# Kernel tuning notes

Hardware: AMD Instinct MI355X
Metric: run time of the kernel (lower is better)

## Reference

```python
import jax, jax.numpy as jnp
import numpy as np

BETA = 0.25


def setup_inputs() -> dict:
    key = jax.random.key(0)
    k1, k2 = jax.random.split(key)
    z = jax.random.normal(k1, (16, 64, 32, 32), dtype=jnp.float32)
    emb_w = jax.random.normal(k2, (16384, 64), dtype=jnp.float32)
    return {"z": z, "emb_w": emb_w}


def reference(z, emb_w):
    # z: [b, c, h, w] with c == embed_dim; emb_w: [n_embed, embed_dim]
    b, c, h, w = z.shape
    zc = jnp.transpose(z, (0, 2, 3, 1))          # [b, h, w, c]
    zf = zc.reshape(-1, c)                        # [N, c]
    # squared euclidean distances: ||z||^2 - 2 z E^T + ||E||^2  -> [N, n_embed]
    d = (jnp.sum(zf * zf, axis=1, keepdims=True)
         - 2.0 * (zf @ emb_w.T)
         + jnp.sum(emb_w * emb_w, axis=1))
    idx = jnp.argmin(d, axis=1)                   # [N]
    z_q = emb_w[idx].reshape(zc.shape)            # [b, h, w, c]
    # commitment loss (codebook side detached, eval-mode forward)
    loss = BETA * jnp.mean((jax.lax.stop_gradient(z_q) - zc) ** 2)
    # straight-through estimator
    z_q_ste = zc + jax.lax.stop_gradient(z_q - zc)
    z_q_out = jnp.transpose(z_q_ste, (0, 3, 1, 2))  # back to bchw
    return (z_q_out, loss)
```

## Files before the change

kernel.cpp:

```cpp
#include <hip/hip_runtime.h>
#include <math.h>

#define NQ      16384
#define NE      16384
#define DIM     64
#define QB      256
#define CS1     8
#define CPB1    (NE / CS1)
#define CPW1    (CPB1 / 4)
#define NT1     (CPW1 / 32)
#define THREADS 256
#define EPS     0.4f

typedef _Float16 half8  __attribute__((ext_vector_type(8)));
typedef float    f32x4  __attribute__((ext_vector_type(4)));
typedef float    f32x16 __attribute__((ext_vector_type(16)));
typedef unsigned int       uint32;
typedef unsigned short     uint16;
typedef unsigned long long uint64;

typedef union { f32x16 v; f32x4 q[4]; } nvec16;

#define W_NORMS   0
#define W_PM1     16384
#define W_PM2     147456
#define W_PG      278528
#define W_FINALG  344064
#define W_RLIST   360448
#define W_COUNT   376832
#define W_LOSSP   376848
#define W_RKEY    377104
#define W_ZH1     409872
#define W_ZH2     934160
#define W_EH1     1458448
#define W_EH2     1982736

__device__ inline uint32 fmono(float f) {
    uint32 u = __float_as_uint(f);
    return (u & 0x80000000u) ? ~u : (u | 0x80000000u);
}

__global__ __launch_bounds__(THREADS)
void vq_prep(const float* __restrict__ z, const float* __restrict__ emb,
             _Float16* __restrict__ zh1, _Float16* __restrict__ zh2,
             _Float16* __restrict__ eh1, _Float16* __restrict__ eh2,
             float* __restrict__ norms, uint32* __restrict__ count) {
    if (blockIdx.x == 0 && threadIdx.x == 0) *count = 0u;
    if (blockIdx.x < 64) {
        int e = blockIdx.x * THREADS + threadIdx.x;
        const float4* row = reinterpret_cast<const float4*>(emb + (size_t)e * DIM);
        float s = 0.f;
#pragma unroll
        for (int i = 0; i < DIM / 4; ++i) {
            float4 v = row[i];
            s = fmaf(v.x, v.x, s); s = fmaf(v.y, v.y, s);
            s = fmaf(v.z, v.z, s); s = fmaf(v.w, v.w, s);
            union { _Float16 h[4]; uint2 u; } p1, p2;
            float f[4] = {-2.f * v.x, -2.f * v.y, -2.f * v.z, -2.f * v.w};
#pragma unroll
            for (int j = 0; j < 4; ++j) {
                _Float16 h1 = (_Float16)f[j];
                p1.h[j] = h1;
                p2.h[j] = (_Float16)(f[j] - (float)h1);
            }
            *reinterpret_cast<uint2*>(eh1 + (size_t)e * DIM + i * 4) = p1.u;
            *reinterpret_cast<uint2*>(eh2 + (size_t)e * DIM + i * 4) = p2.u;
        }
        norms[e] = s;
    } else {
        int n = (blockIdx.x - 64) * THREADS + threadIdx.x;
        const float* zp = z + (size_t)(n >> 10) * 65536 + (n & 1023);
#pragma unroll 8
        for (int c = 0; c < DIM; ++c) {
            float x = zp[(size_t)c * 1024];
            _Float16 h1 = (_Float16)x;
            _Float16 h2 = (_Float16)(x - (float)h1);
            zh1[(size_t)n * DIM + c] = h1;
            zh2[(size_t)n * DIM + c] = h2;
        }
    }
}

#define LOADT(AS, TL) {                                                            \
    const _Float16* _pa = eh1 + (size_t)(cwbase + (TL) * 32 + q31) * DIM + hi8;    \
    AS[0] = *reinterpret_cast<const half8*>(_pa);                                  \
    AS[1] = *reinterpret_cast<const half8*>(_pa + 16);                             \
    AS[2] = *reinterpret_cast<const half8*>(_pa + 32);                             \
    AS[3] = *reinterpret_cast<const half8*>(_pa + 48); }

#define LOADSN(SN, TL) {                                                           \
    _Pragma("unroll")                                                              \
    for (int k = 0; k < 32; ++k) SN[k] = nrm_s[(TL) * 32 + k]; }

#define MKNS(NS, SN) {                                                             \
    _Pragma("unroll")                                                              \
    for (int j = 0; j < 16; ++j)                                                   \
        NS.v[j] = hi ? SN[(j >> 2) * 8 + 4 + (j & 3)] : SN[(j >> 2) * 8 + (j & 3)]; }

#define COMPUTE(AS, NS, TL) {                                                      \
    const uint32 _tid = (uint32)(TL);                                              \
    _Pragma("unroll")                                                              \
    for (int qg = 0; qg < 8; ++qg) {                                               \
        f32x16 acc;                                                                \
        __builtin_amdgcn_s_setprio(1);                                             \
        acc = __builtin_amdgcn_mfma_f32_32x32x16_f16(AS[0], B[qg][0], NS.v, 0, 0, 0); \
        acc = __builtin_amdgcn_mfma_f32_32x32x16_f16(AS[1], B[qg][1], acc,  0, 0, 0); \
        acc = __builtin_amdgcn_mfma_f32_32x32x16_f16(AS[2], B[qg][2], acc,  0, 0, 0); \
        acc = __builtin_amdgcn_mfma_f32_32x32x16_f16(AS[3], B[qg][3], acc,  0, 0, 0); \
        __builtin_amdgcn_s_setprio(0);                                             \
        float u0 = fminf(fminf(acc[0],  acc[1]),  acc[2]);                         \
        float u1 = fminf(fminf(acc[3],  acc[4]),  acc[5]);                         \
        float u2 = fminf(fminf(acc[6],  acc[7]),  acc[8]);                         \
        float u3 = fminf(fminf(acc[9],  acc[10]), acc[11]);                        \
        float u4 = fminf(fminf(acc[12], acc[13]), acc[14]);                        \
        float v  = fminf(fminf(fminf(u0, u1), u2), fminf(fminf(u3, u4), acc[15])); \
        float nm2 = fminf(m2[qg], fmaxf(v, mv[qg]));              \
        bool lt = v < mv[qg];                             \
        mv[qg] = lt ? v : mv[qg];                                                  \
        mi[qg] = lt ? _tid : mi[qg];                                               \
        m2[qg] = nm2;                                                              \
    } }

__global__ __launch_bounds__(THREADS, 2)
void vq_pass1(const _Float16* __restrict__ zh1, const _Float16* __restrict__ eh1,
              const float* __restrict__ norms,
              float* __restrict__ pm1, float* __restrict__ pm2, uint16* __restrict__ pg) {
    __shared__ float  redv[4][QB];
    __shared__ float  red2[4][QB];
    __shared__ uint32 redg[4][QB];

    const int t    = threadIdx.x;
    const int lane = t & 63;
    const int wave = t >> 6;
    const int q31  = lane & 31;
    const int hi   = lane >> 5;
    const int hi8  = hi * 8;
    const int qbase  = blockIdx.x * QB;
    const int cwbase = blockIdx.y * CPB1 + wave * CPW1;

    const float* nrm_s = norms + (size_t)__builtin_amdgcn_readfirstlane(cwbase);

    half8 B[8][4];
#pragma unroll
    for (int qg = 0; qg < 8; ++qg)
#pragma unroll
        for (int kc = 0; kc < 4; ++kc)
            B[qg][kc] = *reinterpret_cast<const half8*>(
                zh1 + (size_t)(qbase + qg * 32 + q31) * DIM + kc * 16 + hi8);

    float  mv[8], m2[8];
    uint32 mi[8];
#pragma unroll
    for (int q = 0; q < 8; ++q) { mv[q] = INFINITY; m2[q] = INFINITY; mi[q] = 0u; }

    half8 A0[4], A1[4];
    float sn0[32], sn1[32];

    LOADT(A0, 0) LOADSN(sn0, 0)
    for (int tb = 0; tb < NT1; tb += 2) {
        LOADT(A1, tb + 1) LOADSN(sn1, tb + 1)
        {
            nvec16 N0; MKNS(N0, sn0)
            COMPUTE(A0, N0, tb)
        }
        int nx = (tb + 2 < NT1) ? tb + 2 : 0;
        LOADT(A0, nx) LOADSN(sn0, nx)
        {
            nvec16 N1; MKNS(N1, sn1)
            COMPUTE(A1, N1, tb + 1)
        }
    }

    uint32 gi[8];
#pragma unroll
    for (int qg = 0; qg < 8; ++qg)
        gi[qg] = ((uint32)(cwbase >> 5) + mi[qg]) * 2u + (uint32)hi;

#pragma unroll
    for (int qg = 0; qg < 8; ++qg) {
        float  ov = __shfl_xor(mv[qg], 32, 64);
        float  o2 = __shfl_xor(m2[qg], 32, 64);
        uint32 og = (uint32)__shfl_xor((int)gi[qg], 32, 64);
        float nm2 = fminf(fminf(m2[qg], o2), fmaxf(mv[qg], ov));
        if (ov < mv[qg] || (ov == mv[qg] && og < gi[qg])) { mv[qg] = ov; gi[qg] = og; }
        m2[qg] = nm2;
    }
    if (lane < 32) {
#pragma unroll
        for (int qg = 0; qg < 8; ++qg) {
            redv[wave][qg * 32 + lane] = mv[qg];
            red2[wave][qg * 32 + lane] = m2[qg];
            redg[wave][qg * 32 + lane] = gi[qg];
        }
    }
    __syncthreads();

    {
        float  bv = redv[0][t], b2 = red2[0][t];
        uint32 bg = redg[0][t];
#pragma unroll
        for (int w = 1; w < 4; ++w) {
            float v = redv[w][t], s2 = red2[w][t];
            float nm2 = fminf(fminf(b2, s2), fmaxf(bv, v));
            if (v < bv) { bv = v; bg = redg[w][t]; }
            b2 = nm2;
        }
        pm1[(size_t)blockIdx.y * NQ + qbase + t] = bv;
        pm2[(size_t)blockIdx.y * NQ + qbase + t] = b2;
        pg [(size_t)blockIdx.y * NQ + qbase + t] = (uint16)bg;
    }
}

__global__ __launch_bounds__(THREADS)
void vq_select(const float* __restrict__ pm1, const float* __restrict__ pm2,
               const uint16* __restrict__ pg,
               uint32* __restrict__ final_g, uint32* __restrict__ rlist,
               uint32* __restrict__ count, uint64* __restrict__ rkey) {
    const int n = blockIdx.x * THREADS + threadIdx.x;
    float M1 = INFINITY, M2 = INFINITY;
    uint32 G = 0u;
#pragma unroll
    for (int s = 0; s < CS1; ++s) {
        float  m1  = pm1[(size_t)s * NQ + n];
        float  m2s = pm2[(size_t)s * NQ + n];
        uint32 g   = (uint32)pg[(size_t)s * NQ + n];
        float nm2 = fminf(fminf(M2, m2s), fmaxf(M1, m1));
        if (m1 < M1) { M1 = m1; G = g; }
        M2 = nm2;
    }
    rkey[n] = ~0ull;
    if (M2 - M1 > EPS) {
        final_g[n] = G;
    } else {
        final_g[n] = 0xFFFFFFFFu;
        uint32 p = atomicAdd(count, 1u);
        rlist[p] = (uint32)n;
    }
}

__global__ __launch_bounds__(THREADS, 2)
void vq_rescue(const _Float16* __restrict__ zh1, const _Float16* __restrict__ zh2,
               const _Float16* __restrict__ eh1, const _Float16* __restrict__ eh2,
               const float* __restrict__ norms,
               const uint32* __restrict__ rlist, const uint32* __restrict__ countp,
               uint64* __restrict__ rkey) {
    __shared__ float  redv[4][128];
    __shared__ uint32 redg[4][128];

    const uint32 count = *countp;
    const uint32 nch   = (count + 127u) >> 7;
    const int t    = threadIdx.x;
    const int lane = t & 63;
    const int wave = t >> 6;
    const int r15  = lane & 15, hk = lane >> 4;
    const int cy   = blockIdx.x & 15;
    const int rcb  = cy * 1024 + wave * 256;

    for (uint32 cx = (uint32)(blockIdx.x >> 4); cx < nch; cx += 32u) {
        half8 B1[8][2], B2[8][2];
#pragma unroll
        for (int qt = 0; qt < 8; ++qt) {
            uint32 j = cx * 128u + (uint32)(qt * 16 + r15);
            uint32 qid = (j < count) ? rlist[j] : 0u;
#pragma unroll
            for (int kc = 0; kc < 2; ++kc) {
                size_t off = (size_t)qid * DIM + kc * 32 + hk * 8;
                B1[qt][kc] = *reinterpret_cast<const half8*>(zh1 + off);
                B2[qt][kc] = *reinterpret_cast<const half8*>(zh2 + off);
            }
        }

        float  mv[8];
        uint32 mi[8];
#pragma unroll
        for (int q = 0; q < 8; ++q) { mv[q] = INFINITY; mi[q] = 0u; }

        half8 a1[2], a2[2];
        f32x4 nc;
        {
            const _Float16* p1 = eh1 + (size_t)(rcb + r15) * DIM + hk * 8;
            const _Float16* p2 = eh2 + (size_t)(rcb + r15) * DIM + hk * 8;
            a1[0] = *reinterpret_cast<const half8*>(p1);
            a1[1] = *reinterpret_cast<const half8*>(p1 + 32);
            a2[0] = *reinterpret_cast<const half8*>(p2);
            a2[1] = *reinterpret_cast<const half8*>(p2 + 32);
            nc = *reinterpret_cast<const f32x4*>(norms + rcb + hk * 4);
        }

#pragma unroll 2
        for (int tile = 0; tile < 16; ++tile) {
            int nt = (tile + 1 < 16) ? tile + 1 : tile;
            half8 b1[2], b2[2];
            f32x4 nn;
            {
                const _Float16* p1 = eh1 + (size_t)(rcb + nt * 16 + r15) * DIM + hk * 8;
                const _Float16* p2 = eh2 + (size_t)(rcb + nt * 16 + r15) * DIM + hk * 8;
                b1[0] = *reinterpret_cast<const half8*>(p1);
                b1[1] = *reinterpret_cast<const half8*>(p1 + 32);
                b2[0] = *reinterpret_cast<const half8*>(p2);
                b2[1] = *reinterpret_cast<const half8*>(p2 + 32);
                nn = *reinterpret_cast<const f32x4*>(norms + rcb + nt * 16 + hk * 4);
            }

            f32x4 acc[8];
            __builtin_amdgcn_s_setprio(1);
#pragma unroll
            for (int qt = 0; qt < 8; ++qt) {
                acc[qt] = __builtin_amdgcn_mfma_f32_16x16x32_f16(a1[0], B1[qt][0], nc,      0, 0, 0);
                acc[qt] = __builtin_amdgcn_mfma_f32_16x16x32_f16(a1[1], B1[qt][1], acc[qt], 0, 0, 0);
                acc[qt] = __builtin_amdgcn_mfma_f32_16x16x32_f16(a1[0], B2[qt][0], acc[qt], 0, 0, 0);
                acc[qt] = __builtin_amdgcn_mfma_f32_16x16x32_f16(a1[1], B2[qt][1], acc[qt], 0, 0, 0);
                acc[qt] = __builtin_amdgcn_mfma_f32_16x16x32_f16(a2[0], B1[qt][0], acc[qt], 0, 0, 0);
                acc[qt] = __builtin_amdgcn_mfma_f32_16x16x32_f16(a2[1], B1[qt][1], acc[qt], 0, 0, 0);
            }
            __builtin_amdgcn_s_setprio(0);

            const uint32 tid = (uint32)tile;
#pragma unroll
            for (int qt = 0; qt < 8; ++qt) {
                float v = fminf(fminf(fminf(acc[qt][0], acc[qt][1]), acc[qt][2]), acc[qt][3]);
                bool lt = v < mv[qt];
                mv[qt] = lt ? v : mv[qt];
                mi[qt] = lt ? tid : mi[qt];
            }
            a1[0] = b1[0]; a1[1] = b1[1];
            a2[0] = b2[0]; a2[1] = b2[1];
            nc = nn;
        }

        uint32 gi[8];
#pragma unroll
        for (int q = 0; q < 8; ++q)
            gi[q] = (uint32)(rcb >> 2) + (mi[q] << 2) + (uint32)hk;
#pragma unroll
        for (int st = 16; st < 64; st <<= 1) {
#pragma unroll
            for (int q = 0; q < 8; ++q) {
                float  ov = __shfl_xor(mv[q], st, 64);
                uint32 og = (uint32)__shfl_xor((int)gi[q], st, 64);
                if (ov < mv[q] || (ov == mv[q] && og < gi[q])) { mv[q] = ov; gi[q] = og; }
            }
        }
        if (lane < 16) {
#pragma unroll
            for (int qt = 0; qt < 8; ++qt) {
                redv[wave][qt * 16 + lane] = mv[qt];
                redg[wave][qt * 16 + lane] = gi[qt];
            }
        }
        __syncthreads();
        if (t < 128) {
            float  bv = redv[0][t];
            uint32 bg = redg[0][t];
#pragma unroll
            for (int w = 1; w < 4; ++w) {
                float v = redv[w][t];
                if (v < bv) { bv = v; bg = redg[w][t]; }
            }
            uint32 j = cx * 128u + (uint32)t;
            if (j < count) {
                uint64 key = ((uint64)fmono(bv) << 32) | (uint64)bg;
                atomicMin(rkey + rlist[j], key);
            }
        }
        __syncthreads();
    }
}

__global__ __launch_bounds__(THREADS)
void vq_finalize(const float* __restrict__ z,
                 const float* __restrict__ emb,
                 const float* __restrict__ norms,
                 const uint32* __restrict__ final_g,
                 const uint64* __restrict__ rkey,
                 float* __restrict__ out,
                 float* __restrict__ lossp) {
    const int t  = threadIdx.x;
    const int ql = t >> 2, p = t & 3;
    const int n  = blockIdx.x * 64 + ql;
    const int c0 = p * 16;

    uint32 bg = final_g[n];
    if (bg == 0xFFFFFFFFu) {
        uint32 c4 = (uint32)(rkey[n] & 0xFFFFFFFFull) * 4u;
        bg = (c4 >> 5) * 2u + ((c4 >> 2) & 1u);
    }
    const int gbase = (int)((bg >> 1) * 32u + (bg & 1u) * 4u);

    const float* zp = z + (size_t)(n >> 10) * 65536 + (n & 1023);
    float zq[16];
#pragma unroll
    for (int c = 0; c < 16; ++c) zq[c] = zp[(size_t)(c0 + c) * 1024];

    float dp[16];
#pragma unroll
    for (int j = 0; j < 16; ++j) {
        int code = gbase + (j & 3) + 8 * (j >> 2);
        const float4* er = reinterpret_cast<const float4*>(emb + (size_t)code * DIM + c0);
        float d = 0.f;
#pragma unroll
        for (int i = 0; i < 4; ++i) {
            float4 e4 = er[i];
            d = fmaf(e4.x, zq[i * 4 + 0], d);
            d = fmaf(e4.y, zq[i * 4 + 1], d);
            d = fmaf(e4.z, zq[i * 4 + 2], d);
            d = fmaf(e4.w, zq[i * 4 + 3], d);
        }
        dp[j] = d;
    }
#pragma unroll
    for (int st = 1; st < 4; st <<= 1) {
#pragma unroll
        for (int j = 0; j < 16; ++j) dp[j] += __shfl_xor(dp[j], st, 64);
    }

    f32x4 nr[4];
#pragma unroll
    for (int k = 0; k < 4; ++k)
        nr[k] = *reinterpret_cast<const f32x4*>(norms + gbase + k * 8);

    float bs = INFINITY;
    uint32 bi = 0u;
#pragma unroll
    for (int j = 0; j < 16; ++j) {
        float s = fmaf(-2.f, dp[j], nr[j >> 2][j & 3]);
        uint32 code = (uint32)(gbase + (j & 3) + 8 * (j >> 2));
        if (s < bs) { bs = s; bi = code; }
    }

    const float* ew = emb + (size_t)bi * DIM + c0;
    float* op = out + (size_t)(n >> 10) * 65536 + (n & 1023);

    float ls = 0.f;
#pragma unroll
    for (int c = 0; c < 16; ++c) {
        float e = ew[c];
        op[(size_t)(c0 + c) * 1024] = e;
        float d = e - zq[c];
        ls = fmaf(d, d, ls);
    }

#pragma unroll
    for (int off = 32; off > 0; off >>= 1) ls += __shfl_down(ls, off, 64);
    __shared__ float wsum[THREADS / 64];
    if ((t & 63) == 0) wsum[t >> 6] = ls;
    __syncthreads();
    if (t == 0) {
        float s = 0.f;
#pragma unroll
        for (int w = 0; w < THREADS / 64; ++w) s += wsum[w];
        lossp[blockIdx.x] = s;
    }
}

__global__ __launch_bounds__(64)
void vq_loss_final(const float* __restrict__ lossp, float* __restrict__ out) {
    float v = 0.f;
#pragma unroll
    for (int k = 0; k < 4; ++k) v += lossp[threadIdx.x + k * 64];
#pragma unroll
    for (int off = 32; off > 0; off >>= 1) v += __shfl_down(v, off, 64);
    if (threadIdx.x == 0)
        out[1048576] = 0.25f * v / 1048576.0f;
}

extern "C" void kernel_launch(void* const* d_in, const int* in_sizes, int n_in,
                              void* d_out, int out_size, void* d_ws, size_t ws_size,
                              hipStream_t stream) {
    const float* z   = (const float*)d_in[0];
    const float* emb = (const float*)d_in[1];
    float* out = (float*)d_out;

    float* ws = (float*)d_ws;
    float*     norms   = ws + W_NORMS;
    float*     pm1     = ws + W_PM1;
    float*     pm2     = ws + W_PM2;
    uint16*    pg      = (uint16*)(ws + W_PG);
    uint32*    final_g = (uint32*)(ws + W_FINALG);
    uint32*    rlist   = (uint32*)(ws + W_RLIST);
    uint32*    count   = (uint32*)(ws + W_COUNT);
    float*     lossp   = ws + W_LOSSP;
    uint64*    rkey    = (uint64*)(ws + W_RKEY);
    _Float16*  zh1     = (_Float16*)(ws + W_ZH1);
    _Float16*  zh2     = (_Float16*)(ws + W_ZH2);
    _Float16*  eh1     = (_Float16*)(ws + W_EH1);
    _Float16*  eh2     = (_Float16*)(ws + W_EH2);

    vq_prep<<<128, THREADS, 0, stream>>>(z, emb, zh1, zh2, eh1, eh2, norms, count);

    dim3 g1(NQ / QB, CS1);
    vq_pass1<<<g1, THREADS, 0, stream>>>(zh1, eh1, norms, pm1, pm2, pg);

    vq_select<<<NQ / THREADS, THREADS, 0, stream>>>(pm1, pm2, pg, final_g, rlist, count, rkey);

    vq_rescue<<<512, THREADS, 0, stream>>>(zh1, zh2, eh1, eh2, norms, rlist, count, rkey);

    vq_finalize<<<NQ / 64, THREADS, 0, stream>>>(z, emb, norms, final_g, rkey, out, lossp);
    vq_loss_final<<<1, 64, 0, stream>>>(lossp, out);
}
```

Baseline: 87.42 us.

## Parallelize prep kernel across 4 threads per row and ping-pong MFMA accumulators

The prep kernel now splits each embedding row and each query vector across four threads, launching 512 blocks instead of 128. Embedding norms are combined with lane shuffles, and z conversions are written as packed 4-half stores instead of scalar half stores. This is meant to raise parallelism and cut the serial per-thread work in prep. In pass1 the eight MFMA chains alternate between two accumulators, so the min-tracking reductions of one chain can overlap the next chain's MFMAs, at the cost of more register pressure.

```diff
diff --git a/kernel.cpp b/kernel.cpp
--- a/kernel.cpp
+++ b/kernel.cpp
@@ -46,12 +46,13 @@
              _Float16* __restrict__ eh1, _Float16* __restrict__ eh2,
              float* __restrict__ norms, uint32* __restrict__ count) {
     if (blockIdx.x == 0 && threadIdx.x == 0) *count = 0u;
-    if (blockIdx.x < 64) {
-        int e = blockIdx.x * THREADS + threadIdx.x;
-        const float4* row = reinterpret_cast<const float4*>(emb + (size_t)e * DIM);
+    if (blockIdx.x < 256) {
+        int gid = blockIdx.x * THREADS + threadIdx.x;
+        int e = gid >> 2, p = gid & 3;
+        const float4* row = reinterpret_cast<const float4*>(emb + (size_t)e * DIM + p * 16);
         float s = 0.f;
 #pragma unroll
-        for (int i = 0; i < DIM / 4; ++i) {
+        for (int i = 0; i < 4; ++i) {
             float4 v = row[i];
             s = fmaf(v.x, v.x, s); s = fmaf(v.y, v.y, s);
             s = fmaf(v.z, v.z, s); s = fmaf(v.w, v.w, s);
@@ -63,20 +64,28 @@
                 p1.h[j] = h1;
                 p2.h[j] = (_Float16)(f[j] - (float)h1);
             }
-            *reinterpret_cast<uint2*>(eh1 + (size_t)e * DIM + i * 4) = p1.u;
-            *reinterpret_cast<uint2*>(eh2 + (size_t)e * DIM + i * 4) = p2.u;
-        }
-        norms[e] = s;
+            *reinterpret_cast<uint2*>(eh1 + (size_t)e * DIM + p * 16 + i * 4) = p1.u;
+            *reinterpret_cast<uint2*>(eh2 + (size_t)e * DIM + p * 16 + i * 4) = p2.u;
+        }
+        s += __shfl_xor(s, 1, 64);
+        s += __shfl_xor(s, 2, 64);
+        if (p == 0) norms[e] = s;
     } else {
-        int n = (blockIdx.x - 64) * THREADS + threadIdx.x;
-        const float* zp = z + (size_t)(n >> 10) * 65536 + (n & 1023);
-#pragma unroll 8
-        for (int c = 0; c < DIM; ++c) {
-            float x = zp[(size_t)c * 1024];
-            _Float16 h1 = (_Float16)x;
-            _Float16 h2 = (_Float16)(x - (float)h1);
-            zh1[(size_t)n * DIM + c] = h1;
-            zh2[(size_t)n * DIM + c] = h2;
+        int gid = (blockIdx.x - 256) * THREADS + threadIdx.x;
+        int n = gid >> 2, p = gid & 3;
+        const float* zp = z + (size_t)(n >> 10) * 65536 + (n & 1023) + (size_t)(p * 16) * 1024;
+#pragma unroll
+        for (int i4 = 0; i4 < 4; ++i4) {
+            union { _Float16 h[4]; uint2 u; } p1, p2;
+#pragma unroll
+            for (int j = 0; j < 4; ++j) {
+                float x = zp[(size_t)(i4 * 4 + j) * 1024];
+                _Float16 h1 = (_Float16)x;
+                p1.h[j] = h1;
+                p2.h[j] = (_Float16)(x - (float)h1);
+            }
+            *reinterpret_cast<uint2*>(zh1 + (size_t)n * DIM + p * 16 + i4 * 4) = p1.u;
+            *reinterpret_cast<uint2*>(zh2 + (size_t)n * DIM + p * 16 + i4 * 4) = p2.u;
         }
     }
 }
@@ -97,29 +106,39 @@
     for (int j = 0; j < 16; ++j)                                                   \
         NS.v[j] = hi ? SN[(j >> 2) * 8 + 4 + (j & 3)] : SN[(j >> 2) * 8 + (j & 3)]; }
 
+#define CHAIN(ACC, AS, NS, QG)                                                     \
+    __builtin_amdgcn_s_setprio(1);                                                 \
+    ACC = __builtin_amdgcn_mfma_f32_32x32x16_f16(AS[0], B[QG][0], NS.v, 0, 0, 0);  \
+    ACC = __builtin_amdgcn_mfma_f32_32x32x16_f16(AS[1], B[QG][1], ACC,  0, 0, 0);  \
+    ACC = __builtin_amdgcn_mfma_f32_32x32x16_f16(AS[2], B[QG][2], ACC,  0, 0, 0);  \
+    ACC = __builtin_amdgcn_mfma_f32_32x32x16_f16(AS[3], B[QG][3], ACC,  0, 0, 0);  \
+    __builtin_amdgcn_s_setprio(0);
+
+#define MINTRK(ACC, QG, TID) {                                                     \
+    float u0 = fminf(fminf(ACC[0],  ACC[1]),  ACC[2]);                             \
+    float u1 = fminf(fminf(ACC[3],  ACC[4]),  ACC[5]);                             \
+    float u2 = fminf(fminf(ACC[6],  ACC[7]),  ACC[8]);                             \
+    float u3 = fminf(fminf(ACC[9],  ACC[10]), ACC[11]);                            \
+    float u4 = fminf(fminf(ACC[12], ACC[13]), ACC[14]);                            \
+    float v  = fminf(fminf(fminf(u0, u1), u2), fminf(fminf(u3, u4), ACC[15]));     \
+    float nm2 = fminf(m2[QG], fmaxf(v, mv[QG]));                  \
+    bool lt = v < mv[QG];                                 \
+    mv[QG] = lt ? v : mv[QG];                                                      \
+    mi[QG] = lt ? (TID) : mi[QG];                                                  \
+    m2[QG] = nm2; }
+
 #define COMPUTE(AS, NS, TL) {                                                      \
     const uint32 _tid = (uint32)(TL);                                              \
-    _Pragma("unroll")                                                              \
-    for (int qg = 0; qg < 8; ++qg) {                                               \
-        f32x16 acc;                                                                \
-        __builtin_amdgcn_s_setprio(1);                                             \
-        acc = __builtin_amdgcn_mfma_f32_32x32x16_f16(AS[0], B[qg][0], NS.v, 0, 0, 0); \
-        acc = __builtin_amdgcn_mfma_f32_32x32x16_f16(AS[1], B[qg][1], acc,  0, 0, 0); \
-        acc = __builtin_amdgcn_mfma_f32_32x32x16_f16(AS[2], B[qg][2], acc,  0, 0, 0); \
-        acc = __builtin_amdgcn_mfma_f32_32x32x16_f16(AS[3], B[qg][3], acc,  0, 0, 0); \
-        __builtin_amdgcn_s_setprio(0);                                             \
-        float u0 = fminf(fminf(acc[0],  acc[1]),  acc[2]);                         \
-        float u1 = fminf(fminf(acc[3],  acc[4]),  acc[5]);                         \
-        float u2 = fminf(fminf(acc[6],  acc[7]),  acc[8]);                         \
-        float u3 = fminf(fminf(acc[9],  acc[10]), acc[11]);                        \
-        float u4 = fminf(fminf(acc[12], acc[13]), acc[14]);                        \
-        float v  = fminf(fminf(fminf(u0, u1), u2), fminf(fminf(u3, u4), acc[15])); \
-        float nm2 = fminf(m2[qg], fmaxf(v, mv[qg]));              \
-        bool lt = v < mv[qg];                             \
-        mv[qg] = lt ? v : mv[qg];                                                  \
-        mi[qg] = lt ? _tid : mi[qg];                                               \
-        m2[qg] = nm2;                                                              \
-    } }
+    f32x16 aA, aB;                                                                 \
+    CHAIN(aA, AS, NS, 0)                                                           \
+    CHAIN(aB, AS, NS, 1) MINTRK(aA, 0, _tid)                                       \
+    CHAIN(aA, AS, NS, 2) MINTRK(aB, 1, _tid)                                       \
+    CHAIN(aB, AS, NS, 3) MINTRK(aA, 2, _tid)                                       \
+    CHAIN(aA, AS, NS, 4) MINTRK(aB, 3, _tid)                                       \
+    CHAIN(aB, AS, NS, 5) MINTRK(aA, 4, _tid)                                       \
+    CHAIN(aA, AS, NS, 6) MINTRK(aB, 5, _tid)                                       \
+    CHAIN(aB, AS, NS, 7) MINTRK(aA, 6, _tid)                                       \
+    MINTRK(aB, 7, _tid) }
 
 __global__ __launch_bounds__(THREADS, 2)
 void vq_pass1(const _Float16* __restrict__ zh1, const _Float16* __restrict__ eh1,
@@ -486,7 +505,7 @@
     _Float16*  eh1     = (_Float16*)(ws + W_EH1);
     _Float16*  eh2     = (_Float16*)(ws + W_EH2);
 
-    vq_prep<<<128, THREADS, 0, stream>>>(z, emb, zh1, zh2, eh1, eh2, norms, count);
+    vq_prep<<<512, THREADS, 0, stream>>>(z, emb, zh1, zh2, eh1, eh2, norms, count);
 
     dim3 g1(NQ / QB, CS1);
     vq_pass1<<<g1, THREADS, 0, stream>>>(zh1, eh1, norms, pm1, pm2, pg);
```

Measured after the change: 98.35 us. +12.5%, slower.
